# Kernel optimization log

Measured on AMD Instinct MI355X. Metric: run time of the kernel, lower is better.

## Reference

```python
import jax, jax.numpy as jnp
import numpy as np

N, E, DIN, DOUT = 10000, 160000, 256, 256
NEG_SLOPE = 0.2
BN_EPS = 1e-5
DROP_P = 0.5


def setup_inputs() -> dict:
    key = jax.random.key(0)
    ks = jax.random.split(key, 12)
    s = 1.0 / np.sqrt(DIN)
    return {
        "x": jax.random.normal(ks[0], (N, DIN), jnp.float32),
        "edge_index": jax.random.randint(ks[1], (2, E), 0, N, jnp.int64),
        "Wl": jax.random.normal(ks[2], (DIN, DOUT), jnp.float32) * s,
        "bl": jax.random.normal(ks[3], (DOUT,), jnp.float32) * s,
        "Wr": jax.random.normal(ks[4], (DIN, DOUT), jnp.float32) * s,
        "br": jax.random.normal(ks[5], (DOUT,), jnp.float32) * s,
        "att": jax.random.normal(ks[6], (DOUT,), jnp.float32) * (1.0 / np.sqrt(DOUT)),
        "bias": jax.random.normal(ks[7], (DOUT,), jnp.float32) * 0.01,
        "gamma": jnp.ones((DOUT,), jnp.float32),
        "beta": jnp.zeros((DOUT,), jnp.float32),
        "dropout_u": jax.random.uniform(ks[8], (N, DOUT), jnp.float32),
    }


def reference(x, edge_index, Wl, bl, Wr, br, att, bias, gamma, beta, dropout_u):
    n = x.shape[0]
    # GATv2Conv (heads=1): separate source/target linear maps
    xl = x @ Wl + bl  # source features [N, DOUT]
    xr = x @ Wr + br  # target features [N, DOUT]
    # add self-loops (PyG default add_self_loops=True)
    loop = jnp.arange(n, dtype=edge_index.dtype)
    src = jnp.concatenate([edge_index[0], loop])  # [E+N]
    dst = jnp.concatenate([edge_index[1], loop])
    # GATv2 attention: e = att . LeakyReLU(xl_j + xr_i)
    h = jax.nn.leaky_relu(xl[src] + xr[dst], NEG_SLOPE)  # [E+N, DOUT]
    alpha = h @ att  # [E+N]
    # segment softmax over destination nodes
    amax = jax.ops.segment_max(alpha, dst, num_segments=n)
    alpha = jnp.exp(alpha - amax[dst])
    denom = jax.ops.segment_sum(alpha, dst, num_segments=n)
    alpha = alpha / denom[dst]
    # scatter-add aggregate of weighted source features
    out = jax.ops.segment_sum(xl[src] * alpha[:, None], dst, num_segments=n)
    out = out + bias
    # ReLU -> dropout(p=0.5, training) -> BatchNorm (training stats)
    out = jax.nn.relu(out)
    mask = (dropout_u >= DROP_P).astype(out.dtype) / (1.0 - DROP_P)
    out = out * mask
    mean = out.mean(axis=0)
    var = out.var(axis=0)  # biased, as BatchNorm uses for normalization
    out = gamma * (out - mean) * jax.lax.rsqrt(var + BN_EPS) + beta
    return out
```

## Files before the change

kernel.cpp:

```cpp
#include <hip/hip_runtime.h>
#include <hip/hip_bf16.h>
#include <math.h>

#define D 256
#define CAP 128
#define NEG_SLOPE 0.2f
#define BN_EPS 1e-5f

typedef __attribute__((ext_vector_type(8))) short bf16x8;
typedef __attribute__((ext_vector_type(8))) unsigned short ushort8;
typedef __attribute__((ext_vector_type(4))) float f32x4;

__device__ inline unsigned short f2bf(float f) {
    union { float f; unsigned u; } v; v.f = f;
    unsigned u = v.u;
    unsigned r = u + 0x7FFFu + ((u >> 16) & 1u);
    return (unsigned short)(r >> 16);
}
__device__ inline float bf2f(unsigned short u) {
    union { unsigned u; float f; } v; v.u = ((unsigned)u) << 16; return v.f;
}

__device__ __forceinline__ void gload16(const void* g, void* l) {
    __builtin_amdgcn_global_load_lds(
        (const __attribute__((address_space(1))) unsigned int*)g,
        (__attribute__((address_space(3))) unsigned int*)l,
        16, 0, 0);
}

__global__ void prep_kernel(const float* __restrict__ X,
                            const float* __restrict__ Wl, const float* __restrict__ Wr,
                            int* __restrict__ zero_base, int nzero,
                            unsigned short* __restrict__ Bt,
                            unsigned short* __restrict__ Xbf, int N) {
    int b = blockIdx.x;
    if (b < 42) {
        int idx = b * 256 + threadIdx.x;
        if (idx < nzero) zero_base[idx] = 0;
    } else if (b < 42 + 512) {
        int n = b - 42;
        int k = threadIdx.x;
        const float* W = (n < 256) ? Wl : Wr;
        int nn = n & 255;
        int ks = k ^ ((n & 7) << 3);
        Bt[(size_t)n * 256 + ks] = f2bf(W[(size_t)k * 256 + nn]);
    } else {
        int idx = (b - 554) * 256 + threadIdx.x;
        int row = idx >> 5;
        int k0 = (idx & 31) * 8;
        int ks = k0 ^ ((row & 7) << 3);
        ushort8 v = {0, 0, 0, 0, 0, 0, 0, 0};
        if (row < N) {
            const float* src = X + (size_t)row * 256 + k0;
            float4 f0 = *(const float4*)(src);
            float4 f1 = *(const float4*)(src + 4);
            v[0] = f2bf(f0.x); v[1] = f2bf(f0.y);
            v[2] = f2bf(f0.z); v[3] = f2bf(f0.w);
            v[4] = f2bf(f1.x); v[5] = f2bf(f1.y);
            v[6] = f2bf(f1.z); v[7] = f2bf(f1.w);
        }
        *(ushort8*)(Xbf + (size_t)row * 256 + ks) = v;
    }
}

__global__ __launch_bounds__(256) void gemm_scatter_kernel(
    const unsigned short* __restrict__ Xbf, const unsigned short* __restrict__ Bt,
    const float* __restrict__ bl, const float* __restrict__ br,
    const int* __restrict__ ei, int* __restrict__ counts, int* __restrict__ ssrc,
    unsigned short* __restrict__ xlbf, float* __restrict__ xr,
    int M, int E, int N, int ngemm)
{
    if ((int)blockIdx.x >= ngemm) {
        int e = (blockIdx.x - ngemm) * 256 + threadIdx.x;
        if (e < E + N) {
            int src, dst;
            if (e < E) { src = ei[e]; dst = ei[E + e]; }
            else       { src = dst = e - E; }
            int pos = atomicAdd(&counts[dst], 1);
            if (pos < CAP) ssrc[dst * CAP + pos] = src;
        }
        return;
    }

    __shared__ __align__(16) unsigned short As[64 * 128];
    __shared__ __align__(16) unsigned short Bs[64 * 128];

    const int tid = threadIdx.x;
    const int wave = tid >> 6, lane = tid & 63;
    const int m_l = lane & 15, quad = lane >> 4;
    const int row0 = (blockIdx.x >> 3) * 64;
    const int n0 = (blockIdx.x & 7) * 64;
    const int sw = (m_l & 7) << 3;

    f32x4 acc[4] = {};

    for (int k0 = 0; k0 < 256; k0 += 128) {
        __syncthreads();
        #pragma unroll
        for (int i = 0; i < 4; i++) {
            int L = (tid + i * 256) * 16;
            int r = L >> 8;
            int cb = L & 255;
            gload16((const char*)Xbf + (size_t)(row0 + r) * 512 + (size_t)k0 * 2 + cb,
                    (char*)As + L);
            gload16((const char*)Bt + (size_t)(n0 + r) * 512 + (size_t)k0 * 2 + cb,
                    (char*)Bs + L);
        }
        __syncthreads();

        #pragma unroll
        for (int kk0 = 0; kk0 < 128; kk0 += 32) {
            int ka = (kk0 + quad * 8) ^ sw;
            bf16x8 a = *(const bf16x8*)&As[(wave * 16 + m_l) * 128 + ka];
            #pragma unroll
            for (int c = 0; c < 4; c++) {
                bf16x8 b = *(const bf16x8*)&Bs[(c * 16 + m_l) * 128 + ka];
                acc[c] = __builtin_amdgcn_mfma_f32_16x16x32_bf16(a, b, acc[c], 0, 0, 0);
            }
        }
    }

    const bool isl = (n0 < 256);
    #pragma unroll
    for (int c = 0; c < 4; c++) {
        int col = n0 + c * 16 + m_l;
        int cc = col & 255;
        float bv = isl ? bl[cc] : br[cc];
        #pragma unroll
        for (int r = 0; r < 4; r++) {
            int row = row0 + wave * 16 + quad * 4 + r;
            if (row < M) {
                float v = acc[c][r] + bv;
                if (isl) xlbf[(size_t)row * 256 + cc] = f2bf(v);
                else     xr[(size_t)row * 256 + cc] = v;
            }
        }
    }
}

__device__ inline float dot8leaky(const float* f, float4 bA, float4 bB,
                                  float4 aA, float4 aB) {
    float h, s = 0.f;
    h = f[0] + bA.x; h = (h > 0.f) ? h : NEG_SLOPE * h; s += h * aA.x;
    h = f[1] + bA.y; h = (h > 0.f) ? h : NEG_SLOPE * h; s += h * aA.y;
    h = f[2] + bA.z; h = (h > 0.f) ? h : NEG_SLOPE * h; s += h * aA.z;
    h = f[3] + bA.w; h = (h > 0.f) ? h : NEG_SLOPE * h; s += h * aA.w;
    h = f[4] + bB.x; h = (h > 0.f) ? h : NEG_SLOPE * h; s += h * aB.x;
    h = f[5] + bB.y; h = (h > 0.f) ? h : NEG_SLOPE * h; s += h * aB.y;
    h = f[6] + bB.z; h = (h > 0.f) ? h : NEG_SLOPE * h; s += h * aB.z;
    h = f[7] + bB.w; h = (h > 0.f) ? h : NEG_SLOPE * h; s += h * aB.w;
    return s;
}

__global__ __launch_bounds__(256) void node_kernel(
    const unsigned short* __restrict__ xlbf, const float* __restrict__ xr,
    const float* __restrict__ att, const float* __restrict__ bias,
    const float* __restrict__ du, const int* __restrict__ counts,
    const int* __restrict__ ssrc, float* __restrict__ out, int N)
{
    const int wave = threadIdx.x >> 6, lane = threadIdx.x & 63;
    const int i = blockIdx.x * 4 + wave;
    if (i >= N) return;
    const int hl = lane & 31;
    const int sid = lane >> 5;

    int cnt = counts[i];
    if (cnt > CAP) cnt = CAP;
    const int start = i * CAP, end = start + cnt;

    int srcv = (lane < cnt) ? ssrc[start + lane] : 0;

    const float4 attA = ((const float4*)att)[hl * 2];
    const float4 attB = ((const float4*)att)[hl * 2 + 1];
    const float4 bA = ((const float4*)(xr + (size_t)i * D))[hl * 2];
    const float4 bB = ((const float4*)(xr + (size_t)i * D))[hl * 2 + 1];

    float m = -INFINITY, lsum = 0.f;
    float acc[8] = {0.f, 0.f, 0.f, 0.f, 0.f, 0.f, 0.f, 0.f};
    const ushort8 z8 = {0, 0, 0, 0, 0, 0, 0, 0};
    const unsigned short* xb = xlbf + hl * 8;

    int e = start + sid;

    if (cnt <= 64) {
        ushort8 p0, p1, p2, p3;
        {
            int o = sid;
            int a0 = __shfl(srcv, o);
            int a1 = __shfl(srcv, o + 2);
            int a2 = __shfl(srcv, o + 4);
            int a3 = __shfl(srcv, o + 6);
            p0 = (e     < end) ? *(const ushort8*)(xb + (size_t)a0 * D) : z8;
            p1 = (e + 2 < end) ? *(const ushort8*)(xb + (size_t)a1 * D) : z8;
            p2 = (e + 4 < end) ? *(const ushort8*)(xb + (size_t)a2 * D) : z8;
            p3 = (e + 6 < end) ? *(const ushort8*)(xb + (size_t)a3 * D) : z8;
        }

        while (e < end) {
            ushort8 c0 = p0, c1 = p1, c2 = p2, c3 = p3;
            bool v1 = (e + 2 < end), v2 = (e + 4 < end), v3 = (e + 6 < end);
            int en = e + 8;
            {
                int on = en - start;
                int a0 = __shfl(srcv, on);
                int a1 = __shfl(srcv, on + 2);
                int a2 = __shfl(srcv, on + 4);
                int a3 = __shfl(srcv, on + 6);
                p0 = (en     < end) ? *(const ushort8*)(xb + (size_t)a0 * D) : z8;
                p1 = (en + 2 < end) ? *(const ushort8*)(xb + (size_t)a1 * D) : z8;
                p2 = (en + 4 < end) ? *(const ushort8*)(xb + (size_t)a2 * D) : z8;
                p3 = (en + 6 < end) ? *(const ushort8*)(xb + (size_t)a3 * D) : z8;
            }

            float f0[8], f1[8], f2[8], f3[8];
            #pragma unroll
            for (int k = 0; k < 8; k++) {
                f0[k] = bf2f(c0[k]); f1[k] = bf2f(c1[k]);
                f2[k] = bf2f(c2[k]); f3[k] = bf2f(c3[k]);
            }

            float s0 = dot8leaky(f0, bA, bB, attA, attB);
            float s1 = dot8leaky(f1, bA, bB, attA, attB);
            float s2 = dot8leaky(f2, bA, bB, attA, attB);
            float s3 = dot8leaky(f3, bA, bB, attA, attB);

            #pragma unroll
            for (int off = 1; off < 32; off <<= 1) {
                s0 += __shfl_xor(s0, off);
                s1 += __shfl_xor(s1, off);
                s2 += __shfl_xor(s2, off);
                s3 += __shfl_xor(s3, off);
            }
            if (!v1) s1 = -INFINITY;
            if (!v2) s2 = -INFINITY;
            if (!v3) s3 = -INFINITY;

            float mnew = fmaxf(fmaxf(m, fmaxf(s0, s1)), fmaxf(s2, s3));
            float sc = __expf(m - mnew);
            float e0e = __expf(s0 - mnew);
            float e1e = __expf(s1 - mnew);
            float e2e = __expf(s2 - mnew);
            float e3e = __expf(s3 - mnew);
            lsum = lsum * sc + e0e + e1e + e2e + e3e;
            #pragma unroll
            for (int k = 0; k < 8; k++) {
                acc[k] = acc[k] * sc + e0e * f0[k] + e1e * f1[k]
                                     + e2e * f2[k] + e3e * f3[k];
            }
            m = mnew;
            e = en;
        }
    } else {
        ushort8 p0, p1, p2, p3;
        p0 = (e     < end) ? *(const ushort8*)(xb + (size_t)ssrc[e]     * D) : z8;
        p1 = (e + 2 < end) ? *(const ushort8*)(xb + (size_t)ssrc[e + 2] * D) : z8;
        p2 = (e + 4 < end) ? *(const ushort8*)(xb + (size_t)ssrc[e + 4] * D) : z8;
        p3 = (e + 6 < end) ? *(const ushort8*)(xb + (size_t)ssrc[e + 6] * D) : z8;

        while (e < end) {
            ushort8 c0 = p0, c1 = p1, c2 = p2, c3 = p3;
            bool v1 = (e + 2 < end), v2 = (e + 4 < end), v3 = (e + 6 < end);
            int en = e + 8;
            p0 = (en     < end) ? *(const ushort8*)(xb + (size_t)ssrc[en]     * D) : z8;
            p1 = (en + 2 < end) ? *(const ushort8*)(xb + (size_t)ssrc[en + 2] * D) : z8;
            p2 = (en + 4 < end) ? *(const ushort8*)(xb + (size_t)ssrc[en + 4] * D) : z8;
            p3 = (en + 6 < end) ? *(const ushort8*)(xb + (size_t)ssrc[en + 6] * D) : z8;

            float f0[8], f1[8], f2[8], f3[8];
            #pragma unroll
            for (int k = 0; k < 8; k++) {
                f0[k] = bf2f(c0[k]); f1[k] = bf2f(c1[k]);
                f2[k] = bf2f(c2[k]); f3[k] = bf2f(c3[k]);
            }

            float s0 = dot8leaky(f0, bA, bB, attA, attB);
            float s1 = dot8leaky(f1, bA, bB, attA, attB);
            float s2 = dot8leaky(f2, bA, bB, attA, attB);
            float s3 = dot8leaky(f3, bA, bB, attA, attB);

            #pragma unroll
            for (int off = 1; off < 32; off <<= 1) {
                s0 += __shfl_xor(s0, off);
                s1 += __shfl_xor(s1, off);
                s2 += __shfl_xor(s2, off);
                s3 += __shfl_xor(s3, off);
            }
            if (!v1) s1 = -INFINITY;
            if (!v2) s2 = -INFINITY;
            if (!v3) s3 = -INFINITY;

            float mnew = fmaxf(fmaxf(m, fmaxf(s0, s1)), fmaxf(s2, s3));
            float sc = __expf(m - mnew);
            float e0e = __expf(s0 - mnew);
            float e1e = __expf(s1 - mnew);
            float e2e = __expf(s2 - mnew);
            float e3e = __expf(s3 - mnew);
            lsum = lsum * sc + e0e + e1e + e2e + e3e;
            #pragma unroll
            for (int k = 0; k < 8; k++) {
                acc[k] = acc[k] * sc + e0e * f0[k] + e1e * f1[k]
                                     + e2e * f2[k] + e3e * f3[k];
            }
            m = mnew;
            e = en;
        }
    }

    {
        float mO = __shfl_xor(m, 32);
        float lO = __shfl_xor(lsum, 32);
        float accO[8];
        #pragma unroll
        for (int k = 0; k < 8; k++) accO[k] = __shfl_xor(acc[k], 32);
        float mn = fmaxf(m, mO);
        float wS = (m  == -INFINITY) ? 0.f : __expf(m - mn);
        float wO = (mO == -INFINITY) ? 0.f : __expf(mO - mn);
        lsum = lsum * wS + lO * wO;
        #pragma unroll
        for (int k = 0; k < 8; k++) acc[k] = acc[k] * wS + accO[k] * wO;
    }

    if (lane < 32) {
        float inv = 1.f / lsum;
        float4 biA = ((const float4*)bias)[hl * 2];
        float4 biB = ((const float4*)bias)[hl * 2 + 1];
        float4 uA = ((const float4*)(du + (size_t)i * D))[hl * 2];
        float4 uB = ((const float4*)(du + (size_t)i * D))[hl * 2 + 1];
        float4 oA, oB;
        oA.x = fmaxf(acc[0] * inv + biA.x, 0.f); oA.x = (uA.x >= 0.5f) ? 2.f * oA.x : 0.f;
        oA.y = fmaxf(acc[1] * inv + biA.y, 0.f); oA.y = (uA.y >= 0.5f) ? 2.f * oA.y : 0.f;
        oA.z = fmaxf(acc[2] * inv + biA.z, 0.f); oA.z = (uA.z >= 0.5f) ? 2.f * oA.z : 0.f;
        oA.w = fmaxf(acc[3] * inv + biA.w, 0.f); oA.w = (uA.w >= 0.5f) ? 2.f * oA.w : 0.f;
        oB.x = fmaxf(acc[4] * inv + biB.x, 0.f); oB.x = (uB.x >= 0.5f) ? 2.f * oB.x : 0.f;
        oB.y = fmaxf(acc[5] * inv + biB.y, 0.f); oB.y = (uB.y >= 0.5f) ? 2.f * oB.y : 0.f;
        oB.z = fmaxf(acc[6] * inv + biB.z, 0.f); oB.z = (uB.z >= 0.5f) ? 2.f * oB.z : 0.f;
        oB.w = fmaxf(acc[7] * inv + biB.w, 0.f); oB.w = (uB.w >= 0.5f) ? 2.f * oB.w : 0.f;
        ((float4*)(out + (size_t)i * D))[hl * 2] = oA;
        ((float4*)(out + (size_t)i * D))[hl * 2 + 1] = oB;
    }
}

__global__ __launch_bounds__(512) void bn_reduce_kernel(const float* __restrict__ pre,
                                 float* __restrict__ colsum,
                                 float* __restrict__ colsumsq, int N) {
    __shared__ float ls[256], ls2[256];
    const int col = threadIdx.x & 255;
    const int team = threadIdx.x >> 8;
    const int S = gridDim.x * 2;
    const int stream = blockIdx.x * 2 + team;
    float s = 0.f, s2 = 0.f;
    int r = stream;
    for (; r + 3 * S < N; r += 4 * S) {
        float v0 = pre[(size_t)r * D + col];
        float v1 = pre[(size_t)(r + S) * D + col];
        float v2 = pre[(size_t)(r + 2 * S) * D + col];
        float v3 = pre[(size_t)(r + 3 * S) * D + col];
        s += v0 + v1 + v2 + v3;
        s2 += v0 * v0 + v1 * v1 + v2 * v2 + v3 * v3;
    }
    for (; r < N; r += S) {
        float v = pre[(size_t)r * D + col];
        s += v; s2 += v * v;
    }
    if (team == 1) { ls[col] = s; ls2[col] = s2; }
    __syncthreads();
    if (team == 0) {
        s += ls[col]; s2 += ls2[col];
        atomicAdd(&colsum[col], s);
        atomicAdd(&colsumsq[col], s2);
    }
}

__global__ void bn_apply_kernel(float* __restrict__ out,
                                const float* __restrict__ colsum,
                                const float* __restrict__ colsumsq,
                                const float* __restrict__ gamma,
                                const float* __restrict__ beta, int N) {
    int idx4 = blockIdx.x * 256 + threadIdx.x;
    int t0 = (idx4 * 4) & (D - 1);
    float invN = 1.f / (float)N;
    float4 v = ((const float4*)out)[idx4];
    float4 o;
    #pragma unroll
    for (int j = 0; j < 4; j++) {
        float mean = colsum[t0 + j] * invN;
        float var = colsumsq[t0 + j] * invN - mean * mean;
        float r = rsqrtf(var + BN_EPS);
        float vv = (j == 0) ? v.x : (j == 1) ? v.y : (j == 2) ? v.z : v.w;
        float oo = gamma[t0 + j] * (vv - mean) * r + beta[t0 + j];
        if (j == 0) o.x = oo; else if (j == 1) o.y = oo; else if (j == 2) o.z = oo; else o.w = oo;
    }
    ((float4*)out)[idx4] = o;
}

extern "C" void kernel_launch(void* const* d_in, const int* in_sizes, int n_in,
                              void* d_out, int out_size, void* d_ws, size_t ws_size,
                              hipStream_t stream) {
    const float* x     = (const float*)d_in[0];
    const int*   ei    = (const int*)d_in[1];
    const float* Wl    = (const float*)d_in[2];
    const float* bl    = (const float*)d_in[3];
    const float* Wr    = (const float*)d_in[4];
    const float* br    = (const float*)d_in[5];
    const float* att   = (const float*)d_in[6];
    const float* bias  = (const float*)d_in[7];
    const float* gamma = (const float*)d_in[8];
    const float* beta  = (const float*)d_in[9];
    const float* du    = (const float*)d_in[10];

    const int N = in_sizes[0] / D;
    const int E = in_sizes[1] / 2;
    const int Mpad = (N + 63) & ~63;

    int* ws = (int*)d_ws;
    size_t off = 0;
    float* xr       = (float*)(ws + off); off += (size_t)N * D;
    unsigned short* xlbf = (unsigned short*)(ws + off); off += (size_t)N * D / 2;
    unsigned short* Xbf  = (unsigned short*)(ws + off); off += (size_t)Mpad * D / 2;
    unsigned short* Bt   = (unsigned short*)(ws + off); off += 512 * 256 / 2;
    int*   ssrc     = ws + off;           off += (size_t)N * CAP;
    float* colsum   = (float*)(ws + off); off += D;
    float* colsumsq = (float*)(ws + off); off += D;
    int*   counts   = ws + off;           off += N;
    int nzero = 2 * D + N;

    int nconv = (Mpad * 32) / 256;
    prep_kernel<<<42 + 512 + nconv, 256, 0, stream>>>(
        x, Wl, Wr, (int*)colsum, nzero, Bt, Xbf, N);

    int nMtiles = (N + 63) / 64;
    int ngemm = nMtiles * 8;
    int nscat = (E + N + 255) / 256;
    gemm_scatter_kernel<<<ngemm + nscat, 256, 0, stream>>>(
        Xbf, Bt, bl, br, ei, counts, ssrc, xlbf, xr, N, E, N, ngemm);

    node_kernel<<<(N + 3) / 4, 256, 0, stream>>>(
        xlbf, xr, att, bias, du, counts, ssrc, (float*)d_out, N);

    bn_reduce_kernel<<<128, 512, 0, stream>>>((const float*)d_out, colsum, colsumsq, N);
    bn_apply_kernel<<<(N * D / 4 + 255) / 256, 256, 0, stream>>>(
        (float*)d_out, colsum, colsumsq, gamma, beta, N);
}
```

Measured before the change: 148.7 us.

## Fuse BatchNorm column statistics into node kernel with bucketed atomics

Moves the BatchNorm sum and sum-of-squares reduction into the node kernel's epilogue. Each block reduces its four rows through shared memory and atomically adds into one of 64 bucketed partial-sum arrays, so the separate pass that re-reads the whole output is removed. The apply kernel sums the buckets, precomputes a per-column scale and shift in shared memory, and walks rows in a grid-stride loop. The cost is a block-wide barrier and about 512 atomics per node block, plus a larger zeroing region in the prep kernel.

```diff
diff --git a/kernel.cpp b/kernel.cpp
--- a/kernel.cpp
+++ b/kernel.cpp
@@ -6,6 +6,7 @@
 #define CAP 128
 #define NEG_SLOPE 0.2f
 #define BN_EPS 1e-5f
+#define NBKT 64
 
 typedef __attribute__((ext_vector_type(8))) short bf16x8;
 typedef __attribute__((ext_vector_type(8))) unsigned short ushort8;
@@ -30,22 +31,22 @@
 
 __global__ void prep_kernel(const float* __restrict__ X,
                             const float* __restrict__ Wl, const float* __restrict__ Wr,
-                            int* __restrict__ zero_base, int nzero,
+                            int* __restrict__ zero_base, int nzero, int nzb,
                             unsigned short* __restrict__ Bt,
                             unsigned short* __restrict__ Xbf, int N) {
     int b = blockIdx.x;
-    if (b < 42) {
+    if (b < nzb) {
         int idx = b * 256 + threadIdx.x;
         if (idx < nzero) zero_base[idx] = 0;
-    } else if (b < 42 + 512) {
-        int n = b - 42;
+    } else if (b < nzb + 512) {
+        int n = b - nzb;
         int k = threadIdx.x;
         const float* W = (n < 256) ? Wl : Wr;
         int nn = n & 255;
         int ks = k ^ ((n & 7) << 3);
         Bt[(size_t)n * 256 + ks] = f2bf(W[(size_t)k * 256 + nn]);
     } else {
-        int idx = (b - 554) * 256 + threadIdx.x;
+        int idx = (b - nzb - 512) * 256 + threadIdx.x;
         int row = idx >> 5;
         int k0 = (idx & 31) * 8;
         int ks = k0 ^ ((row & 7) << 3);
@@ -156,15 +157,18 @@
     const unsigned short* __restrict__ xlbf, const float* __restrict__ xr,
     const float* __restrict__ att, const float* __restrict__ bias,
     const float* __restrict__ du, const int* __restrict__ counts,
-    const int* __restrict__ ssrc, float* __restrict__ out, int N)
+    const int* __restrict__ ssrc, float* __restrict__ out,
+    float* __restrict__ bsum, float* __restrict__ bsq, int N)
 {
+    __shared__ float ls[4][256];
+
     const int wave = threadIdx.x >> 6, lane = threadIdx.x & 63;
     const int i = blockIdx.x * 4 + wave;
-    if (i >= N) return;
+    const bool valid = (i < N);
     const int hl = lane & 31;
     const int sid = lane >> 5;
 
-    int cnt = counts[i];
+    int cnt = valid ? counts[i] : 0;
     if (cnt > CAP) cnt = CAP;
     const int start = i * CAP, end = start + cnt;
 
@@ -172,8 +176,9 @@
 
     const float4 attA = ((const float4*)att)[hl * 2];
     const float4 attB = ((const float4*)att)[hl * 2 + 1];
-    const float4 bA = ((const float4*)(xr + (size_t)i * D))[hl * 2];
-    const float4 bB = ((const float4*)(xr + (size_t)i * D))[hl * 2 + 1];
+    const float4 zf4 = {0.f, 0.f, 0.f, 0.f};
+    const float4 bA = valid ? ((const float4*)(xr + (size_t)i * D))[hl * 2] : zf4;
+    const float4 bB = valid ? ((const float4*)(xr + (size_t)i * D))[hl * 2 + 1] : zf4;
 
     float m = -INFINITY, lsum = 0.f;
     float acc[8] = {0.f, 0.f, 0.f, 0.f, 0.f, 0.f, 0.f, 0.f};
@@ -320,77 +325,87 @@
         for (int k = 0; k < 8; k++) acc[k] = acc[k] * wS + accO[k] * wO;
     }
 
+    float ov[8];
     if (lane < 32) {
-        float inv = 1.f / lsum;
-        float4 biA = ((const float4*)bias)[hl * 2];
-        float4 biB = ((const float4*)bias)[hl * 2 + 1];
-        float4 uA = ((const float4*)(du + (size_t)i * D))[hl * 2];
-        float4 uB = ((const float4*)(du + (size_t)i * D))[hl * 2 + 1];
-        float4 oA, oB;
-        oA.x = fmaxf(acc[0] * inv + biA.x, 0.f); oA.x = (uA.x >= 0.5f) ? 2.f * oA.x : 0.f;
-        oA.y = fmaxf(acc[1] * inv + biA.y, 0.f); oA.y = (uA.y >= 0.5f) ? 2.f * oA.y : 0.f;
-        oA.z = fmaxf(acc[2] * inv + biA.z, 0.f); oA.z = (uA.z >= 0.5f) ? 2.f * oA.z : 0.f;
-        oA.w = fmaxf(acc[3] * inv + biA.w, 0.f); oA.w = (uA.w >= 0.5f) ? 2.f * oA.w : 0.f;
-        oB.x = fmaxf(acc[4] * inv + biB.x, 0.f); oB.x = (uB.x >= 0.5f) ? 2.f * oB.x : 0.f;
-        oB.y = fmaxf(acc[5] * inv + biB.y, 0.f); oB.y = (uB.y >= 0.5f) ? 2.f * oB.y : 0.f;
-        oB.z = fmaxf(acc[6] * inv + biB.z, 0.f); oB.z = (uB.z >= 0.5f) ? 2.f * oB.z : 0.f;
-        oB.w = fmaxf(acc[7] * inv + biB.w, 0.f); oB.w = (uB.w >= 0.5f) ? 2.f * oB.w : 0.f;
-        ((float4*)(out + (size_t)i * D))[hl * 2] = oA;
-        ((float4*)(out + (size_t)i * D))[hl * 2 + 1] = oB;
-    }
-}
-
-__global__ __launch_bounds__(512) void bn_reduce_kernel(const float* __restrict__ pre,
-                                 float* __restrict__ colsum,
-                                 float* __restrict__ colsumsq, int N) {
-    __shared__ float ls[256], ls2[256];
-    const int col = threadIdx.x & 255;
-    const int team = threadIdx.x >> 8;
-    const int S = gridDim.x * 2;
-    const int stream = blockIdx.x * 2 + team;
+        if (valid) {
+            float inv = 1.f / lsum;
+            float4 biA = ((const float4*)bias)[hl * 2];
+            float4 biB = ((const float4*)bias)[hl * 2 + 1];
+            float4 uA = ((const float4*)(du + (size_t)i * D))[hl * 2];
+            float4 uB = ((const float4*)(du + (size_t)i * D))[hl * 2 + 1];
+            float4 oA, oB;
+            oA.x = fmaxf(acc[0] * inv + biA.x, 0.f); oA.x = (uA.x >= 0.5f) ? 2.f * oA.x : 0.f;
+            oA.y = fmaxf(acc[1] * inv + biA.y, 0.f); oA.y = (uA.y >= 0.5f) ? 2.f * oA.y : 0.f;
+            oA.z = fmaxf(acc[2] * inv + biA.z, 0.f); oA.z = (uA.z >= 0.5f) ? 2.f * oA.z : 0.f;
+            oA.w = fmaxf(acc[3] * inv + biA.w, 0.f); oA.w = (uA.w >= 0.5f) ? 2.f * oA.w : 0.f;
+            oB.x = fmaxf(acc[4] * inv + biB.x, 0.f); oB.x = (uB.x >= 0.5f) ? 2.f * oB.x : 0.f;
+            oB.y = fmaxf(acc[5] * inv + biB.y, 0.f); oB.y = (uB.y >= 0.5f) ? 2.f * oB.y : 0.f;
+            oB.z = fmaxf(acc[6] * inv + biB.z, 0.f); oB.z = (uB.z >= 0.5f) ? 2.f * oB.z : 0.f;
+            oB.w = fmaxf(acc[7] * inv + biB.w, 0.f); oB.w = (uB.w >= 0.5f) ? 2.f * oB.w : 0.f;
+            ((float4*)(out + (size_t)i * D))[hl * 2] = oA;
+            ((float4*)(out + (size_t)i * D))[hl * 2 + 1] = oB;
+            ov[0] = oA.x; ov[1] = oA.y; ov[2] = oA.z; ov[3] = oA.w;
+            ov[4] = oB.x; ov[5] = oB.y; ov[6] = oB.z; ov[7] = oB.w;
+        } else {
+            #pragma unroll
+            for (int k = 0; k < 8; k++) ov[k] = 0.f;
+        }
+        #pragma unroll
+        for (int k = 0; k < 8; k++) ls[wave][hl * 8 + k] = ov[k];
+    }
+    __syncthreads();
+
+    {
+        int t = threadIdx.x;
+        float s = 0.f, s2 = 0.f;
+        #pragma unroll
+        for (int w = 0; w < 4; w++) {
+            float v = ls[w][t];
+            s += v; s2 += v * v;
+        }
+        int bkt = (blockIdx.x & (NBKT - 1)) * 256 + t;
+        atomicAdd(&bsum[bkt], s);
+        atomicAdd(&bsq[bkt], s2);
+    }
+}
+
+__global__ __launch_bounds__(256) void bn_apply_kernel(
+    float* __restrict__ out,
+    const float* __restrict__ bsum, const float* __restrict__ bsq,
+    const float* __restrict__ gamma, const float* __restrict__ beta, int N)
+{
+    __shared__ float scaleL[256], shiftL[256];
+    const int t = threadIdx.x;
     float s = 0.f, s2 = 0.f;
-    int r = stream;
-    for (; r + 3 * S < N; r += 4 * S) {
-        float v0 = pre[(size_t)r * D + col];
-        float v1 = pre[(size_t)(r + S) * D + col];
-        float v2 = pre[(size_t)(r + 2 * S) * D + col];
-        float v3 = pre[(size_t)(r + 3 * S) * D + col];
-        s += v0 + v1 + v2 + v3;
-        s2 += v0 * v0 + v1 * v1 + v2 * v2 + v3 * v3;
-    }
-    for (; r < N; r += S) {
-        float v = pre[(size_t)r * D + col];
-        s += v; s2 += v * v;
-    }
-    if (team == 1) { ls[col] = s; ls2[col] = s2; }
+    #pragma unroll 8
+    for (int b = 0; b < NBKT; b++) {
+        s += bsum[b * 256 + t];
+        s2 += bsq[b * 256 + t];
+    }
+    float invN = 1.f / (float)N;
+    float mean = s * invN;
+    float var = s2 * invN - mean * mean;
+    float rs = rsqrtf(var + BN_EPS);
+    float sc = gamma[t] * rs;
+    scaleL[t] = sc;
+    shiftL[t] = beta[t] - mean * sc;
     __syncthreads();
-    if (team == 0) {
-        s += ls[col]; s2 += ls2[col];
-        atomicAdd(&colsum[col], s);
-        atomicAdd(&colsumsq[col], s2);
-    }
-}
-
-__global__ void bn_apply_kernel(float* __restrict__ out,
-                                const float* __restrict__ colsum,
-                                const float* __restrict__ colsumsq,
-                                const float* __restrict__ gamma,
-                                const float* __restrict__ beta, int N) {
-    int idx4 = blockIdx.x * 256 + threadIdx.x;
-    int t0 = (idx4 * 4) & (D - 1);
-    float invN = 1.f / (float)N;
-    float4 v = ((const float4*)out)[idx4];
-    float4 o;
-    #pragma unroll
-    for (int j = 0; j < 4; j++) {
-        float mean = colsum[t0 + j] * invN;
-        float var = colsumsq[t0 + j] * invN - mean * mean;
-        float r = rsqrtf(var + BN_EPS);
-        float vv = (j == 0) ? v.x : (j == 1) ? v.y : (j == 2) ? v.z : v.w;
-        float oo = gamma[t0 + j] * (vv - mean) * r + beta[t0 + j];
-        if (j == 0) o.x = oo; else if (j == 1) o.y = oo; else if (j == 2) o.z = oo; else o.w = oo;
-    }
-    ((float4*)out)[idx4] = o;
+
+    const int c4 = t & 63;
+    float4 scv, shv;
+    scv.x = scaleL[c4 * 4];     shv.x = shiftL[c4 * 4];
+    scv.y = scaleL[c4 * 4 + 1]; shv.y = shiftL[c4 * 4 + 1];
+    scv.z = scaleL[c4 * 4 + 2]; shv.z = shiftL[c4 * 4 + 2];
+    scv.w = scaleL[c4 * 4 + 3]; shv.w = shiftL[c4 * 4 + 3];
+
+    for (int row = blockIdx.x * 4 + (t >> 6); row < N; row += gridDim.x * 4) {
+        float4 v = ((float4*)(out + (size_t)row * D))[c4];
+        v.x = v.x * scv.x + shv.x;
+        v.y = v.y * scv.y + shv.y;
+        v.z = v.z * scv.z + shv.z;
+        v.w = v.w * scv.w + shv.w;
+        ((float4*)(out + (size_t)row * D))[c4] = v;
+    }
 }
 
 extern "C" void kernel_launch(void* const* d_in, const int* in_sizes, int n_in,
@@ -419,14 +434,15 @@
     unsigned short* Xbf  = (unsigned short*)(ws + off); off += (size_t)Mpad * D / 2;
     unsigned short* Bt   = (unsigned short*)(ws + off); off += 512 * 256 / 2;
     int*   ssrc     = ws + off;           off += (size_t)N * CAP;
-    float* colsum   = (float*)(ws + off); off += D;
-    float* colsumsq = (float*)(ws + off); off += D;
+    float* bsum     = (float*)(ws + off); off += NBKT * 256;
+    float* bsq      = (float*)(ws + off); off += NBKT * 256;
     int*   counts   = ws + off;           off += N;
-    int nzero = 2 * D + N;
+    int nzero = 2 * NBKT * 256 + N;
+    int nzb = (nzero + 255) / 256;
 
     int nconv = (Mpad * 32) / 256;
-    prep_kernel<<<42 + 512 + nconv, 256, 0, stream>>>(
-        x, Wl, Wr, (int*)colsum, nzero, Bt, Xbf, N);
+    prep_kernel<<<nzb + 512 + nconv, 256, 0, stream>>>(
+        x, Wl, Wr, (int*)bsum, nzero, nzb, Bt, Xbf, N);
 
     int nMtiles = (N + 63) / 64;
     int ngemm = nMtiles * 8;
@@ -435,9 +451,8 @@
         Xbf, Bt, bl, br, ei, counts, ssrc, xlbf, xr, N, E, N, ngemm);
 
     node_kernel<<<(N + 3) / 4, 256, 0, stream>>>(
-        xlbf, xr, att, bias, du, counts, ssrc, (float*)d_out, N);
-
-    bn_reduce_kernel<<<128, 512, 0, stream>>>((const float*)d_out, colsum, colsumsq, N);
-    bn_apply_kernel<<<(N * D / 4 + 255) / 256, 256, 0, stream>>>(
-        (float*)d_out, colsum, colsumsq, gamma, beta, N);
-}
+        xlbf, xr, att, bias, du, counts, ssrc, (float*)d_out, bsum, bsq, N);
+
+    bn_apply_kernel<<<256, 256, 0, stream>>>(
+        (float*)d_out, bsum, bsq, gamma, beta, N);
+}
```

After: 143.3 us. -3.6%, faster.
